# Performance work log

Hardware: AMD Instinct MI355X
Metric: run time of the kernel (lower is better)

## Reference

```python
import jax, jax.numpy as jnp
import numpy as np

N = 100000
E = 1600000
D = 128

NEG_SLOPE = 0.1


def _leaky(x):
    return jnp.where(x >= 0, x, NEG_SLOPE * x)


def _ising_gcn(x, row, col, val, n, W=None, b=None, bias=None):
    # scatter_mean of |val| over source rows -> custom diagonal
    abs_val = jnp.abs(val)
    cnt = jax.ops.segment_sum(jnp.ones_like(abs_val), row, num_segments=n)
    abs_mean = jax.ops.segment_sum(abs_val, row, num_segments=n) / jnp.maximum(cnt, 1.0)
    diag = jnp.arange(n, dtype=row.dtype)
    frow = jnp.concatenate([row, diag])
    fcol = jnp.concatenate([col, diag])
    fval = jnp.concatenate([val, abs_mean])
    # symmetric normalization on |values|: v / sqrt(deg[row] * deg[col])
    deg = jax.ops.segment_sum(jnp.abs(fval), frow, num_segments=n)
    dinv = jnp.where(deg > 0, jax.lax.rsqrt(deg), 0.0)
    pv = fval * dinv[frow] * dinv[fcol]
    if W is not None:
        x = x @ W.T + b
    # propagate: out[col] += pv * x[row]  (PyG source_to_target, aggr='add')
    out = jax.ops.segment_sum(pv[:, None] * x[frow], fcol, num_segments=n)
    if bias is not None:
        out = out + bias
    return out


def setup_inputs() -> dict:
    key = jax.random.key(0)
    ks = jax.random.split(key, 10)
    edge_index = jax.random.randint(ks[0], (2, E), 0, N, dtype=jnp.int64)
    edge_val = jax.random.normal(ks[1], (E,), dtype=jnp.float32)
    s1 = 1.0 / np.sqrt(1.0)
    s2 = 1.0 / np.sqrt(D)
    s3 = 1.0 / np.sqrt(2 * D)
    return {
        "edge_index": edge_index,
        "edge_val": edge_val,
        "n_nodes": N,
        "w1": jax.random.uniform(ks[2], (D, 1), jnp.float32, -s1, s1),
        "b1": jax.random.uniform(ks[3], (D,), jnp.float32, -s1, s1),
        "w2": jax.random.uniform(ks[4], (2 * D, D), jnp.float32, -s2, s2),
        "b2": jax.random.uniform(ks[5], (2 * D,), jnp.float32, -s2, s2),
        "bias2": jnp.zeros((2 * D,), jnp.float32),
        "w3": jax.random.uniform(ks[6], (D, 2 * D), jnp.float32, -s3, s3),
        "b3": jax.random.uniform(ks[7], (D,), jnp.float32, -s3, s3),
        "bias3": jnp.zeros((D,), jnp.float32),
    }


def reference(edge_index, edge_val, n_nodes, w1, b1, w2, b2, bias2, w3, b3, bias3):
    row, col = edge_index[0], edge_index[1]
    x = jnp.ones((n_nodes, 1), dtype=edge_val.dtype)
    # conv1: no W, no bias (1 -> 1)
    x = _ising_gcn(x, row, col, edge_val, n_nodes)
    # linear 1 -> D, leaky relu (dropout omitted: inference)
    x = _leaky(x @ w1.T + b1)
    # conv2: D -> 2D with lin + bias
    x = _leaky(_ising_gcn(x, row, col, edge_val, n_nodes, W=w2, b=b2, bias=bias2))
    # conv3: 2D -> D with lin + bias
    x = _leaky(_ising_gcn(x, row, col, edge_val, n_nodes, W=w3, b=b3, bias=bias3))
    return x
```

## Files before the change

kernel.cpp:

```cpp
#include <hip/hip_runtime.h>
#include <hip/hip_bf16.h>

#define NEG_SLOPE 0.1f
#define D1 128
#define D2 256

#define BSH 7
#define NPB 128
#define EPB 2048
#define MAXBUK 1024

__device__ __forceinline__ float leaky(float x) { return x >= 0.f ? x : NEG_SLOPE * x; }

__device__ __forceinline__ unsigned short f2bf(float x) {
    union { float f; unsigned int u; } v; v.f = x;
    unsigned int r = (v.u + 0x7FFFu + ((v.u >> 16) & 1u)) >> 16;
    return (unsigned short)r;
}

__device__ __forceinline__ unsigned int pk2bf(float a, float b) {
    return (unsigned int)f2bf(a) | ((unsigned int)f2bf(b) << 16);
}

__device__ __forceinline__ int ts_g(const int* __restrict__ TS,
                                    const int* __restrict__ partials, int idx) {
    return TS[idx] + partials[idx >> 11];
}

__global__ __launch_bounds__(256) void k_hist(const int* __restrict__ row,
                                              const int* __restrict__ col,
                                              int* __restrict__ T,
                                              int E, int NBLK, int NBUK)
{
    __shared__ int hc[MAXBUK], hr[MAXBUK];
    for (int b = threadIdx.x; b < NBUK; b += 256) { hc[b] = 0; hr[b] = 0; }
    __syncthreads();
    int base = blockIdx.x * EPB;
#pragma unroll
    for (int i = 0; i < 8; i++) {
        int e = base + i * 256 + threadIdx.x;
        if (e < E) {
            atomicAdd(&hc[col[e] >> BSH], 1);
            atomicAdd(&hr[row[e] >> BSH], 1);
        }
    }
    __syncthreads();
    int NT = NBUK * NBLK;
    for (int b = threadIdx.x; b < NBUK; b += 256) {
        T[b * NBLK + blockIdx.x]      = hc[b];
        T[NT + b * NBLK + blockIdx.x] = hr[b];
    }
}

__global__ __launch_bounds__(256) void k_scan_local(const int* __restrict__ in, int* __restrict__ out,
                                                    int* __restrict__ partials, int n)
{
    __shared__ int s[256];
    int base = blockIdx.x * 2048 + threadIdx.x * 8;
    int v[8]; int sum = 0;
#pragma unroll
    for (int i = 0; i < 8; i++) { v[i] = (base + i < n) ? in[base + i] : 0; sum += v[i]; }
    s[threadIdx.x] = sum;
    __syncthreads();
    for (int off = 1; off < 256; off <<= 1) {
        int t = (threadIdx.x >= off) ? s[threadIdx.x - off] : 0;
        __syncthreads();
        s[threadIdx.x] += t;
        __syncthreads();
    }
    int excl = s[threadIdx.x] - sum;
#pragma unroll
    for (int i = 0; i < 8; i++) { if (base + i < n) { out[base + i] = excl; excl += v[i]; } }
    if (threadIdx.x == 255) partials[blockIdx.x] = s[255];
}

__global__ __launch_bounds__(1024) void k_scan_cvt(int* __restrict__ partials, int nb,
                                                   const float* __restrict__ w2,
                                                   const float* __restrict__ w3,
                                                   unsigned short* __restrict__ w2f,
                                                   unsigned short* __restrict__ w3f)
{
    int t = threadIdx.x;
    if (blockIdx.x == 0) {
        __shared__ int s[1024];
        int v = (t < nb) ? partials[t] : 0;
        s[t] = v;
        __syncthreads();
        for (int off = 1; off < 1024; off <<= 1) {
            int u = (t >= off) ? s[t - off] : 0;
            __syncthreads();
            s[t] += u;
            __syncthreads();
        }
        if (t < nb) partials[t] = s[t] - v;
    } else {
        int i = (blockIdx.x - 1) * 1024 + t;
        {
            int m = i >> 7, k = i & 127;
            w2f[(((k >> 3) * 256 + m) << 3) + (k & 7)] = f2bf(w2[i]);
        }
        {
            int m = i >> 8, k = i & 255;
            w3f[(((k >> 3) * 128 + m) << 3) + (k & 7)] = f2bf(w3[i]);
        }
    }
}

__global__ __launch_bounds__(256) void k_scat(const int* __restrict__ row,
                                              const int* __restrict__ col,
                                              const float* __restrict__ val,
                                              const int* __restrict__ TS,
                                              const int* __restrict__ partials,
                                              int2* __restrict__ X, int2* __restrict__ Y,
                                              int E, int NBLK, int NBUK)
{
    __shared__ int oc[MAXBUK], orw[MAXBUK];
    int NT = NBUK * NBLK;
    for (int b = threadIdx.x; b < NBUK; b += 256) {
        oc[b]  = ts_g(TS, partials, b * NBLK + blockIdx.x);
        orw[b] = ts_g(TS, partials, NT + b * NBLK + blockIdx.x);
    }
    __syncthreads();
    int base = blockIdx.x * EPB;
#pragma unroll
    for (int i = 0; i < 8; i++) {
        int e = base + i * 256 + threadIdx.x;
        if (e < E) {
            int r = row[e], c = col[e];
            float v = val[e];
            int pc = atomicAdd(&oc[c >> BSH], 1);
            X[pc] = make_int2(((c & (NPB - 1)) << 25) | r, __float_as_int(v));
            int pr = atomicAdd(&orw[r >> BSH], 1);
            Y[pr - E] = make_int2(r & (NPB - 1), __float_as_int(fabsf(v)));
        }
    }
}

__global__ __launch_bounds__(256) void k_rowstats(const int2* __restrict__ Y,
                                                  const int* __restrict__ TS,
                                                  const int* __restrict__ partials,
                                                  float* __restrict__ dinv,
                                                  float* __restrict__ pv_self,
                                                  int N, int E, int NBLK, int NBUK)
{
    __shared__ float fs[NPB];
    __shared__ int   cn[NPB];
    int t = threadIdx.x;
    if (t < NPB) { fs[t] = 0.f; cn[t] = 0; }
    __syncthreads();
    int NT = NBUK * NBLK;
    int buk = blockIdx.x;
    int s = ts_g(TS, partials, NT + buk * NBLK);
    int e = (buk == NBUK - 1) ? 2 * E : ts_g(TS, partials, NT + (buk + 1) * NBLK);
    for (int j = s + t; j < e; j += 256) {
        int2 y = Y[j - E];
        atomicAdd(&fs[y.x], __int_as_float(y.y));
        atomicAdd(&cn[y.x], 1);
    }
    __syncthreads();
    if (t < NPB) {
        int node = buk * NPB + t;
        if (node < N) {
            float as = fs[t];
            float c  = (float)cn[t];
            float am = as / fmaxf(c, 1.f);
            float deg = as + am;
            float di = deg > 0.f ? rsqrtf(deg) : 0.f;
            dinv[node]    = di;
            pv_self[node] = am * di * di;
        }
    }
}

__global__ __launch_bounds__(256) void k_colfinal(const int2* __restrict__ X,
                                                  const int* __restrict__ TS,
                                                  const int* __restrict__ partials,
                                                  const float* __restrict__ dinv,
                                                  const float* __restrict__ pv_self,
                                                  int* __restrict__ col_ptr,
                                                  int2* __restrict__ srt_rp,
                                                  float* __restrict__ x1,
                                                  int N, int E, int NBLK, int NBUK)
{
    __shared__ int   hist[NPB];
    __shared__ int   tmp[NPB];
    __shared__ int   rb[NPB];
    __shared__ float xs[NPB];
    __shared__ float dl[NPB];
    int t = threadIdx.x;
    int buk = blockIdx.x;
    int node = buk * NPB + t;
    if (t < NPB) {
        hist[t] = 0; xs[t] = 0.f;
        dl[t] = (node < N) ? dinv[node] : 0.f;
    }
    __syncthreads();
    int s  = ts_g(TS, partials, buk * NBLK);
    int e2 = (buk == NBUK - 1) ? E : ts_g(TS, partials, (buk + 1) * NBLK);
    for (int j = s + t; j < e2; j += 256) {
        unsigned xw = (unsigned)X[j].x;
        atomicAdd(&hist[xw >> 25], 1);
    }
    __syncthreads();
    if (t < NPB) tmp[t] = hist[t];
    __syncthreads();
    for (int off = 1; off < NPB; off <<= 1) {
        int u = (t >= off && t < NPB) ? tmp[t - off] : 0;
        __syncthreads();
        if (t < NPB) tmp[t] += u;
        __syncthreads();
    }
    if (t < NPB) {
        int excl = tmp[t] - hist[t];
        rb[t] = s + excl;
        if (node < N) col_ptr[node] = s + excl;
    }
    if (buk == NBUK - 1 && t == 0) col_ptr[N] = E;
    __syncthreads();
    for (int j = s + t; j < e2; j += 256) {
        int2 xx = X[j];
        unsigned xw = (unsigned)xx.x;
        int cl = xw >> 25;
        int r  = (int)(xw & 0x1FFFFFFu);
        float p = __int_as_float(xx.y) * dinv[r] * dl[cl];
        int pos = atomicAdd(&rb[cl], 1);
        srt_rp[pos] = make_int2(r, __float_as_int(p));
        atomicAdd(&xs[cl], p);
    }
    __syncthreads();
    if (t < NPB && node < N) x1[node] = pv_self[node] + xs[t];
}

__global__ __launch_bounds__(256) void k_prop2b(const int* __restrict__ col_ptr,
                                                const int2* __restrict__ srt_rp,
                                                const float* __restrict__ pv_self,
                                                const float* __restrict__ x1,
                                                const float* __restrict__ w1,
                                                const float* __restrict__ b1,
                                                unsigned int* __restrict__ p2b, int N)
{
    int node = blockIdx.x * 4 + (threadIdx.x >> 6);
    int lane = threadIdx.x & 63;
    if (node >= N) return;

    float2 w = *(const float2*)&w1[lane * 2];
    float2 b = *(const float2*)&b1[lane * 2];
    float ps  = pv_self[node];
    float x1n = x1[node];
    float acc0 = ps * leaky(fmaf(x1n, w.x, b.x));
    float acc1 = ps * leaky(fmaf(x1n, w.y, b.y));

    int s = col_ptr[node], e = col_ptr[node + 1];
    for (int base = s; base < e; base += 64) {
        int mc = min(64, e - base);
        float p = 0.f, sv = 0.f;
        if (lane < mc) {
            int2 rp = srt_rp[base + lane];
            p  = __int_as_float(rp.y);
            sv = x1[rp.x];
        }
        for (int k = 0; k < mc; ++k) {
            float pk = __shfl(p, k, 64);
            float sk = __shfl(sv, k, 64);
            acc0 += pk * leaky(fmaf(sk, w.x, b.x));
            acc1 += pk * leaky(fmaf(sk, w.y, b.y));
        }
    }

    p2b[(size_t)node * 64 + lane] = pk2bf(acc0, acc1);
}

__global__ __launch_bounds__(256) void k_prop3_bf16(const int* __restrict__ col_ptr,
                                                    const int2* __restrict__ srt_rp,
                                                    const float* __restrict__ pv_self,
                                                    const unsigned int* __restrict__ zb,
                                                    const float* __restrict__ bias3,
                                                    float* __restrict__ out, int N)
{
    int node = blockIdx.x * 4 + (threadIdx.x >> 6);
    int lane = threadIdx.x & 63;
    if (node >= N) return;

    unsigned int us = zb[(size_t)node * 64 + lane];
    float ps = pv_self[node];
    float acc0 = ps * __uint_as_float(us << 16);
    float acc1 = ps * __uint_as_float(us & 0xFFFF0000u);

    int j = col_ptr[node], e = col_ptr[node + 1];
    for (; j + 3 < e; j += 4) {
        int2 rp0 = srt_rp[j];
        int2 rp1 = srt_rp[j + 1];
        int2 rp2 = srt_rp[j + 2];
        int2 rp3 = srt_rp[j + 3];
        unsigned int u0 = zb[(size_t)rp0.x * 64 + lane];
        unsigned int u1 = zb[(size_t)rp1.x * 64 + lane];
        unsigned int u2 = zb[(size_t)rp2.x * 64 + lane];
        unsigned int u3 = zb[(size_t)rp3.x * 64 + lane];
        float p0 = __int_as_float(rp0.y);
        float p1 = __int_as_float(rp1.y);
        float p2 = __int_as_float(rp2.y);
        float p3 = __int_as_float(rp3.y);
        acc0 += p0 * __uint_as_float(u0 << 16);
        acc1 += p0 * __uint_as_float(u0 & 0xFFFF0000u);
        acc0 += p1 * __uint_as_float(u1 << 16);
        acc1 += p1 * __uint_as_float(u1 & 0xFFFF0000u);
        acc0 += p2 * __uint_as_float(u2 << 16);
        acc1 += p2 * __uint_as_float(u2 & 0xFFFF0000u);
        acc0 += p3 * __uint_as_float(u3 << 16);
        acc1 += p3 * __uint_as_float(u3 & 0xFFFF0000u);
    }
    for (; j < e; ++j) {
        int2 rp = srt_rp[j];
        unsigned int u = zb[(size_t)rp.x * 64 + lane];
        float p = __int_as_float(rp.y);
        acc0 += p * __uint_as_float(u << 16);
        acc1 += p * __uint_as_float(u & 0xFFFF0000u);
    }

    float2 b = *(const float2*)&bias3[lane * 2];
    float2 o = make_float2(leaky(acc0 + b.x), leaky(acc1 + b.y));
    *(float2*)&out[(size_t)node * D1 + lane * 2] = o;
}

__global__ __launch_bounds__(256, 4) void k_gemm_fused3(const unsigned int* __restrict__ p2b,
                                                        const unsigned short* __restrict__ w2f,
                                                        const float* __restrict__ b2,
                                                        const float* __restrict__ bias2,
                                                        const unsigned short* __restrict__ w3f,
                                                        const float* __restrict__ b3,
                                                        const float* __restrict__ x1,
                                                        unsigned short* __restrict__ zb,
                                                        int N)
{
    typedef __attribute__((ext_vector_type(8))) short short8v;
    typedef __attribute__((ext_vector_type(4))) float f32x4;

    __shared__ unsigned short H[32 * 64 * 8];

    const int t = threadIdx.x;
    const int n_base = blockIdx.x * 64;
    const int l  = t & 63, wid = t >> 6;
    const int lr = l & 15, lk = l >> 4;

    f32x4 acc1[4][4] = {};
#pragma unroll
    for (int k0 = 0; k0 < D1; k0 += 32) {
        short8v af[4], bf[4];
#pragma unroll
        for (int i = 0; i < 4; i++)
            af[i] = *(const short8v*)&w2f[((((k0 >> 3) + lk) * 256) + wid * 64 + i * 16 + lr) * 8];
#pragma unroll
        for (int j = 0; j < 4; j++) {
            int node = n_base + j * 16 + lr;
            if (node < N)
                bf[j] = *(const short8v*)&p2b[(size_t)node * 64 + (k0 >> 1) + lk * 4];
            else
                bf[j] = short8v{0, 0, 0, 0, 0, 0, 0, 0};
        }
#pragma unroll
        for (int i = 0; i < 4; i++)
#pragma unroll
            for (int j = 0; j < 4; j++)
                acc1[i][j] = __builtin_amdgcn_mfma_f32_16x16x32_bf16(af[i], bf[j], acc1[i][j], 0, 0, 0);
    }

    {
        float xv[4];
#pragma unroll
        for (int j = 0; j < 4; j++) {
            int node = n_base + j * 16 + lr;
            xv[j] = (node < N) ? x1[node] : 0.f;
        }
#pragma unroll
        for (int i = 0; i < 4; i++) {
            const int c0 = wid * 64 + i * 16 + lk * 4;
            float4 bq  = *(const float4*)&b2[c0];
            float4 biq = *(const float4*)&bias2[c0];
            const int kblk = wid * 8 + i * 2 + (lk >> 1);
#pragma unroll
            for (int j = 0; j < 4; j++) {
                float v0 = leaky(acc1[i][j][0] + xv[j] * bq.x + biq.x);
                float v1 = leaky(acc1[i][j][1] + xv[j] * bq.y + biq.y);
                float v2 = leaky(acc1[i][j][2] + xv[j] * bq.z + biq.z);
                float v3 = leaky(acc1[i][j][3] + xv[j] * bq.w + biq.w);
                uint2 pk = make_uint2(pk2bf(v0, v1), pk2bf(v2, v3));
                *(uint2*)&H[(kblk * 64 + j * 16 + lr) * 8 + (lk & 1) * 4] = pk;
            }
        }
    }
    __syncthreads();

    f32x4 acc2[2][4] = {};
#pragma unroll
    for (int k0 = 0; k0 < D2; k0 += 32) {
        short8v af[2], bf[4];
#pragma unroll
        for (int i = 0; i < 2; i++)
            af[i] = *(const short8v*)&w3f[((((k0 >> 3) + lk) * 128) + wid * 32 + i * 16 + lr) * 8];
#pragma unroll
        for (int j = 0; j < 4; j++)
            bf[j] = *(const short8v*)&H[(((k0 >> 3) + lk) * 64 + j * 16 + lr) * 8];
#pragma unroll
        for (int i = 0; i < 2; i++)
#pragma unroll
            for (int j = 0; j < 4; j++)
                acc2[i][j] = __builtin_amdgcn_mfma_f32_16x16x32_bf16(af[i], bf[j], acc2[i][j], 0, 0, 0);
    }

#pragma unroll
    for (int i = 0; i < 2; i++) {
        const int m0 = wid * 32 + i * 16 + lk * 4;
        float4 bq = *(const float4*)&b3[m0];
#pragma unroll
        for (int j = 0; j < 4; j++) {
            int node = n_base + j * 16 + lr;
            if (node < N) {
                ushort4 s4;
                s4.x = f2bf(acc2[i][j][0] + bq.x);
                s4.y = f2bf(acc2[i][j][1] + bq.y);
                s4.z = f2bf(acc2[i][j][2] + bq.z);
                s4.w = f2bf(acc2[i][j][3] + bq.w);
                *(ushort4*)&zb[(size_t)node * D1 + m0] = s4;
            }
        }
    }
}

extern "C" void kernel_launch(void* const* d_in, const int* in_sizes, int n_in,
                              void* d_out, int out_size, void* d_ws, size_t ws_size,
                              hipStream_t stream)
{
    const int* ei       = (const int*)d_in[0];
    const float* val    = (const float*)d_in[1];
    const float* w1     = (const float*)d_in[3];
    const float* b1     = (const float*)d_in[4];
    const float* w2     = (const float*)d_in[5];
    const float* b2     = (const float*)d_in[6];
    const float* bias2  = (const float*)d_in[7];
    const float* w3     = (const float*)d_in[8];
    const float* b3     = (const float*)d_in[9];
    const float* bias3  = (const float*)d_in[10];
    float* out = (float*)d_out;

    const int E = in_sizes[1];
    const int N = out_size / D1;
    const int* row = ei;
    const int* col = ei + E;

    const int NBLK = (E + EPB - 1) / EPB;
    const int NBUK = (N + NPB - 1) >> BSH;
    const int NT   = NBUK * NBLK;

    float* dinv    = (float*)d_ws;
    float* pv_self = dinv + N;
    float* x1      = pv_self + N;
    int*   col_ptr = (int*)(x1 + N);
    int*   partials= col_ptr + N + 8;
    int2*  srt_rp  = (int2*)(partials + 1024);
    unsigned int* p2b = (unsigned int*)(srt_rp + (size_t)E);
    int*   TS      = (int*)(p2b + (size_t)N * 64);
    int*   T       = TS + (size_t)2 * NT;
    int2*  Y       = (int2*)(T + (size_t)2 * NT);
    unsigned short* w2f = (unsigned short*)(Y + (size_t)E);
    unsigned short* w3f = w2f + 32768;
    int2* X = (int2*)p2b;
    unsigned short* zb = (unsigned short*)p2b;

    const int B = 256;
    const int n2 = 2 * NT;
    const int scan_blocks = (n2 + 2047) / 2048;

    k_hist<<<NBLK, B, 0, stream>>>(row, col, T, E, NBLK, NBUK);
    k_scan_local<<<scan_blocks, 256, 0, stream>>>(T, TS, partials, n2);
    k_scan_cvt<<<33, 1024, 0, stream>>>(partials, scan_blocks, w2, w3, w2f, w3f);
    k_scat<<<NBLK, B, 0, stream>>>(row, col, val, TS, partials, X, Y, E, NBLK, NBUK);
    k_rowstats<<<NBUK, B, 0, stream>>>(Y, TS, partials, dinv, pv_self, N, E, NBLK, NBUK);
    k_colfinal<<<NBUK, B, 0, stream>>>(X, TS, partials, dinv, pv_self, col_ptr, srt_rp, x1, N, E, NBLK, NBUK);

    k_prop2b<<<(N + 3) / 4, 256, 0, stream>>>(col_ptr, srt_rp, pv_self, x1, w1, b1, p2b, N);
    k_gemm_fused3<<<(N + 63) / 64, 256, 0, stream>>>(p2b, w2f, b2, bias2, w3f, b3, x1, zb, N);

    k_prop3_bf16<<<(N + 3) / 4, 256, 0, stream>>>(col_ptr, srt_rp, pv_self, (const unsigned int*)zb, bias3, out, N);
}
```

Baseline: 371.5 us.

## Prefetch all GEMM operands into registers and enlarge edges per block

The fused GEMM kernel now loads every A and B fragment for the first GEMM, and all weight fragments for the second GEMM, into registers before issuing MFMAs. This is meant to expose memory-level parallelism and hide load latency. It lowers the occupancy hint to 2 blocks per SM to leave room for the larger register footprint, and replaces zero-filling of out-of-range rows with clamped loads. Separately, the histogram and scatter kernels process 8192 edges per block instead of 2048, which cuts block count and the per-block histogram and offset tables in exchange for less parallelism.

```diff
diff --git a/kernel.cpp b/kernel.cpp
--- a/kernel.cpp
+++ b/kernel.cpp
@@ -7,7 +7,7 @@
 
 #define BSH 7
 #define NPB 128
-#define EPB 2048
+#define EPB 8192
 #define MAXBUK 1024
 
 __device__ __forceinline__ float leaky(float x) { return x >= 0.f ? x : NEG_SLOPE * x; }
@@ -36,8 +36,8 @@
     for (int b = threadIdx.x; b < NBUK; b += 256) { hc[b] = 0; hr[b] = 0; }
     __syncthreads();
     int base = blockIdx.x * EPB;
-#pragma unroll
-    for (int i = 0; i < 8; i++) {
+#pragma unroll 8
+    for (int i = 0; i < EPB / 256; i++) {
         int e = base + i * 256 + threadIdx.x;
         if (e < E) {
             atomicAdd(&hc[col[e] >> BSH], 1);
@@ -122,8 +122,8 @@
     }
     __syncthreads();
     int base = blockIdx.x * EPB;
-#pragma unroll
-    for (int i = 0; i < 8; i++) {
+#pragma unroll 8
+    for (int i = 0; i < EPB / 256; i++) {
         int e = base + i * 256 + threadIdx.x;
         if (e < E) {
             int r = row[e], c = col[e];
@@ -322,7 +322,7 @@
     *(float2*)&out[(size_t)node * D1 + lane * 2] = o;
 }
 
-__global__ __launch_bounds__(256, 4) void k_gemm_fused3(const unsigned int* __restrict__ p2b,
+__global__ __launch_bounds__(256, 2) void k_gemm_fused4(const unsigned int* __restrict__ p2b,
                                                         const unsigned short* __restrict__ w2f,
                                                         const float* __restrict__ b2,
                                                         const float* __restrict__ bias2,
@@ -342,26 +342,37 @@
     const int l  = t & 63, wid = t >> 6;
     const int lr = l & 15, lk = l >> 4;
 
-    f32x4 acc1[4][4] = {};
-#pragma unroll
-    for (int k0 = 0; k0 < D1; k0 += 32) {
-        short8v af[4], bf[4];
+    short8v a1[4][4], p1[4][4];
+#pragma unroll
+    for (int ks = 0; ks < 4; ks++) {
+        const int k0 = ks * 32;
 #pragma unroll
         for (int i = 0; i < 4; i++)
-            af[i] = *(const short8v*)&w2f[((((k0 >> 3) + lk) * 256) + wid * 64 + i * 16 + lr) * 8];
+            a1[ks][i] = *(const short8v*)&w2f[((((k0 >> 3) + lk) * 256) + wid * 64 + i * 16 + lr) * 8];
 #pragma unroll
         for (int j = 0; j < 4; j++) {
             int node = n_base + j * 16 + lr;
-            if (node < N)
-                bf[j] = *(const short8v*)&p2b[(size_t)node * 64 + (k0 >> 1) + lk * 4];
-            else
-                bf[j] = short8v{0, 0, 0, 0, 0, 0, 0, 0};
-        }
+            if (node >= N) node = N - 1;
+            p1[ks][j] = *(const short8v*)&p2b[(size_t)node * 64 + (k0 >> 1) + lk * 4];
+        }
+    }
+
+    f32x4 acc1[4][4] = {};
+#pragma unroll
+    for (int ks = 0; ks < 4; ks++)
 #pragma unroll
         for (int i = 0; i < 4; i++)
 #pragma unroll
             for (int j = 0; j < 4; j++)
-                acc1[i][j] = __builtin_amdgcn_mfma_f32_16x16x32_bf16(af[i], bf[j], acc1[i][j], 0, 0, 0);
+                acc1[i][j] = __builtin_amdgcn_mfma_f32_16x16x32_bf16(a1[ks][i], p1[ks][j], acc1[i][j], 0, 0, 0);
+
+    short8v a2[8][2];
+#pragma unroll
+    for (int ks = 0; ks < 8; ks++) {
+        const int k0 = ks * 32;
+#pragma unroll
+        for (int i = 0; i < 2; i++)
+            a2[ks][i] = *(const short8v*)&w3f[((((k0 >> 3) + lk) * 128) + wid * 32 + i * 16 + lr) * 8];
     }
 
     {
@@ -392,11 +403,9 @@
 
     f32x4 acc2[2][4] = {};
 #pragma unroll
-    for (int k0 = 0; k0 < D2; k0 += 32) {
-        short8v af[2], bf[4];
-#pragma unroll
-        for (int i = 0; i < 2; i++)
-            af[i] = *(const short8v*)&w3f[((((k0 >> 3) + lk) * 128) + wid * 32 + i * 16 + lr) * 8];
+    for (int ks = 0; ks < 8; ks++) {
+        const int k0 = ks * 32;
+        short8v bf[4];
 #pragma unroll
         for (int j = 0; j < 4; j++)
             bf[j] = *(const short8v*)&H[(((k0 >> 3) + lk) * 64 + j * 16 + lr) * 8];
@@ -404,7 +413,7 @@
         for (int i = 0; i < 2; i++)
 #pragma unroll
             for (int j = 0; j < 4; j++)
-                acc2[i][j] = __builtin_amdgcn_mfma_f32_16x16x32_bf16(af[i], bf[j], acc2[i][j], 0, 0, 0);
+                acc2[i][j] = __builtin_amdgcn_mfma_f32_16x16x32_bf16(a2[ks][i], bf[j], acc2[i][j], 0, 0, 0);
     }
 
 #pragma unroll
@@ -478,7 +487,7 @@
     k_colfinal<<<NBUK, B, 0, stream>>>(X, TS, partials, dinv, pv_self, col_ptr, srt_rp, x1, N, E, NBLK, NBUK);
 
     k_prop2b<<<(N + 3) / 4, 256, 0, stream>>>(col_ptr, srt_rp, pv_self, x1, w1, b1, p2b, N);
-    k_gemm_fused3<<<(N + 63) / 64, 256, 0, stream>>>(p2b, w2f, b2, bias2, w3f, b3, x1, zb, N);
+    k_gemm_fused4<<<(N + 63) / 64, 256, 0, stream>>>(p2b, w2f, b2, bias2, w3f, b3, x1, zb, N);
 
     k_prop3_bf16<<<(N + 3) / 4, 256, 0, stream>>>(col_ptr, srt_rp, pv_self, (const unsigned int*)zb, bias3, out, N);
 }
```

New measurement: 360.0 us. 3.1% less time.
